# Kernel tuning notes

Hardware: AMD Instinct MI355X
Metric: run time of the kernel (lower is better)

Reference implementation:

```python
import jax, jax.numpy as jnp
import numpy as np

HIDDEN = 1024
HEADS = 16
HEAD_DIM = HIDDEN // HEADS


def setup_inputs() -> dict:
    key = jax.random.key(0)
    ks = jax.random.split(key, 8)
    B, S = 4, 2048
    scale = 1.0 / np.sqrt(HIDDEN)
    return {
        "hidden_states": jax.random.normal(ks[0], (B, S, HIDDEN), dtype=jnp.float32),
        "attention_mask": jnp.zeros((B, 1, 1, S), dtype=jnp.float32),
        "Wq": jax.random.normal(ks[1], (HIDDEN, HIDDEN), dtype=jnp.float32) * scale,
        "bq": jnp.zeros((HIDDEN,), dtype=jnp.float32),
        "Wk": jax.random.normal(ks[2], (HIDDEN, HIDDEN), dtype=jnp.float32) * scale,
        "bk": jnp.zeros((HIDDEN,), dtype=jnp.float32),
        "Wv": jax.random.normal(ks[3], (HIDDEN, HIDDEN), dtype=jnp.float32) * scale,
        "bv": jnp.zeros((HIDDEN,), dtype=jnp.float32),
    }


def _split_heads(x):
    # [B, S, H] -> [B, heads, S, d]
    B, S, _ = x.shape
    return x.reshape(B, S, HEADS, HEAD_DIM).transpose(0, 2, 1, 3)


def reference(hidden_states, attention_mask, Wq, bq, Wk, bk, Wv, bv):
    # nn.Linear: y = x @ W.T + b
    q = _split_heads(hidden_states @ Wq.T + bq)
    k = _split_heads(hidden_states @ Wk.T + bk)
    v = _split_heads(hidden_states @ Wv.T + bv)
    scores = jnp.einsum("bhqd,bhkd->bhqk", q, k) / np.sqrt(HEAD_DIM)
    scores = scores + attention_mask  # additive broadcast mask
    probs = jax.nn.softmax(scores, axis=-1)
    # dropout is identity in eval mode (deterministic reference)
    ctx = jnp.einsum("bhqk,bhkd->bhqd", probs, v)
    B, _, S, _ = ctx.shape
    ctx = ctx.transpose(0, 2, 1, 3).reshape(B, S, HIDDEN)
    return ctx, probs
```

## Files before the change

kernel.cpp:

```cpp
#include <hip/hip_runtime.h>
#include <cstdint>
#include <cstddef>


#define BB 4
#define SS 2048
#define HID 1024
#define NH 16
#define HD 64
#define MTOT (BB * SS)
#define BH (BB * NH)

__global__ __launch_bounds__(256) void qkv_gemm(const float* __restrict__ X,
                                                const float* __restrict__ W,
                                                const float* __restrict__ bias,
                                                float* __restrict__ out) {
    __shared__ float As[16][68];
    __shared__ float Bs[16][68];
    const int t  = threadIdx.x;
    const int m0 = blockIdx.y * 64;
    const int n0 = blockIdx.x * 64;
    const int lr = t >> 2;
    const int lc = (t & 3) * 4;
    const int tr = (t >> 4) * 4;
    const int tc = (t & 15) * 4;

    float acc[4][4];
#pragma unroll
    for (int u = 0; u < 4; u++)
#pragma unroll
        for (int v = 0; v < 4; v++) acc[u][v] = 0.f;

    const float* Xp = X + (size_t)(m0 + lr) * HID + lc;
    const float* Wp = W + (size_t)(n0 + lr) * HID + lc;

    for (int k0 = 0; k0 < HID; k0 += 16) {
        float4 a = *(const float4*)(Xp + k0);
        float4 b = *(const float4*)(Wp + k0);
        __syncthreads();
        As[lc + 0][lr] = a.x; As[lc + 1][lr] = a.y; As[lc + 2][lr] = a.z; As[lc + 3][lr] = a.w;
        Bs[lc + 0][lr] = b.x; Bs[lc + 1][lr] = b.y; Bs[lc + 2][lr] = b.z; Bs[lc + 3][lr] = b.w;
        __syncthreads();
#pragma unroll
        for (int kk = 0; kk < 16; kk++) {
            float4 av = *(const float4*)&As[kk][tr];
            float4 bv = *(const float4*)&Bs[kk][tc];
            acc[0][0] += av.x * bv.x; acc[0][1] += av.x * bv.y; acc[0][2] += av.x * bv.z; acc[0][3] += av.x * bv.w;
            acc[1][0] += av.y * bv.x; acc[1][1] += av.y * bv.y; acc[1][2] += av.y * bv.z; acc[1][3] += av.y * bv.w;
            acc[2][0] += av.z * bv.x; acc[2][1] += av.z * bv.y; acc[2][2] += av.z * bv.z; acc[2][3] += av.z * bv.w;
            acc[3][0] += av.w * bv.x; acc[3][1] += av.w * bv.y; acc[3][2] += av.w * bv.z; acc[3][3] += av.w * bv.w;
        }
    }

    const int n_base = n0 + tc;
    const int h  = n_base >> 6;
    const int d0 = n_base & 63;
    const float4 bvec = *(const float4*)&bias[n_base];
#pragma unroll
    for (int u = 0; u < 4; u++) {
        const int m = m0 + tr + u;
        const int bb = m >> 11;
        const int s  = m & (SS - 1);
        float4 r;
        r.x = acc[u][0] + bvec.x; r.y = acc[u][1] + bvec.y;
        r.z = acc[u][2] + bvec.z; r.w = acc[u][3] + bvec.w;
        *(float4*)&out[((size_t)(bb * NH + h) * SS + s) * HD + d0] = r;
    }
}

__global__ __launch_bounds__(256) void attn(const float* __restrict__ Q,
                                            const float* __restrict__ K,
                                            const float* __restrict__ V,
                                            const float* __restrict__ mask,
                                            float* __restrict__ probs,
                                            float* __restrict__ ctx,
                                            float* __restrict__ invZ) {
    const int bh = blockIdx.x;
    const int q0 = blockIdx.y * 32;
    const int b  = bh >> 4;
    const int h  = bh & 15;
    const int t  = threadIdx.x;

    __shared__ float q_lds[32][68];
    __shared__ float kT[64][68];
    __shared__ float v_lds[64][68];
    __shared__ float e_lds[32][68];
    __shared__ float m_lds[64];

    {
        const int r = t >> 3, c0 = (t & 7) * 8;
        const float* gq = Q + ((size_t)bh * SS + q0 + r) * HD + c0;
        *(float4*)&q_lds[r][c0]     = *(const float4*)gq;
        *(float4*)&q_lds[r][c0 + 4] = *(const float4*)(gq + 4);
    }

    const int i  = t >> 3;
    const int jc = (t & 7) * 4;

    float ctx_acc[8];
#pragma unroll
    for (int u = 0; u < 8; u++) ctx_acc[u] = 0.f;
    float Zpart = 0.f;

    const float* Kb    = K + (size_t)bh * SS * HD;
    const float* Vb    = V + (size_t)bh * SS * HD;
    const float* maskb = mask + (size_t)b * SS;
    float* probs_row   = probs + ((size_t)bh * SS + q0 + i) * SS;

    const int lr = t >> 2;
    const int lc0 = (t & 3) * 16;

    for (int kt = 0; kt < SS; kt += 64) {
        __syncthreads();
        {
            const float* kg = Kb + (size_t)(kt + lr) * HD + lc0;
            const float* vg = Vb + (size_t)(kt + lr) * HD + lc0;
#pragma unroll
            for (int ii = 0; ii < 4; ii++) {
                float4 kx = *(const float4*)(kg + ii * 4);
                kT[lc0 + ii * 4 + 0][lr] = kx.x;
                kT[lc0 + ii * 4 + 1][lr] = kx.y;
                kT[lc0 + ii * 4 + 2][lr] = kx.z;
                kT[lc0 + ii * 4 + 3][lr] = kx.w;
                *(float4*)&v_lds[lr][lc0 + ii * 4] = *(const float4*)(vg + ii * 4);
            }
            if (t < 64) m_lds[t] = maskb[kt + t];
        }
        __syncthreads();

        float sA[4] = {0.f, 0.f, 0.f, 0.f}, sB[4] = {0.f, 0.f, 0.f, 0.f};
#pragma unroll 8
        for (int c = 0; c < 64; c++) {
            const float qv = q_lds[i][c];
            const float4 ka = *(const float4*)&kT[c][jc];
            const float4 kb = *(const float4*)&kT[c][jc + 32];
            sA[0] += qv * ka.x; sA[1] += qv * ka.y; sA[2] += qv * ka.z; sA[3] += qv * ka.w;
            sB[0] += qv * kb.x; sB[1] += qv * kb.y; sB[2] += qv * kb.z; sB[3] += qv * kb.w;
        }
        float4 eA, eB;
        eA.x = __expf(sA[0] * 0.125f + m_lds[jc + 0]);
        eA.y = __expf(sA[1] * 0.125f + m_lds[jc + 1]);
        eA.z = __expf(sA[2] * 0.125f + m_lds[jc + 2]);
        eA.w = __expf(sA[3] * 0.125f + m_lds[jc + 3]);
        eB.x = __expf(sB[0] * 0.125f + m_lds[jc + 32]);
        eB.y = __expf(sB[1] * 0.125f + m_lds[jc + 33]);
        eB.z = __expf(sB[2] * 0.125f + m_lds[jc + 34]);
        eB.w = __expf(sB[3] * 0.125f + m_lds[jc + 35]);
        Zpart += eA.x + eA.y + eA.z + eA.w + eB.x + eB.y + eB.z + eB.w;
        *(float4*)&e_lds[i][jc]      = eA;
        *(float4*)&e_lds[i][jc + 32] = eB;
        *(float4*)(probs_row + kt + jc)      = eA;
        *(float4*)(probs_row + kt + jc + 32) = eB;
        __syncthreads();

#pragma unroll 8
        for (int j = 0; j < 64; j++) {
            const float ev = e_lds[i][j];
            const float4 va = *(const float4*)&v_lds[j][jc];
            const float4 vb = *(const float4*)&v_lds[j][jc + 32];
            ctx_acc[0] += ev * va.x; ctx_acc[1] += ev * va.y; ctx_acc[2] += ev * va.z; ctx_acc[3] += ev * va.w;
            ctx_acc[4] += ev * vb.x; ctx_acc[5] += ev * vb.y; ctx_acc[6] += ev * vb.z; ctx_acc[7] += ev * vb.w;
        }
    }

    Zpart += __shfl_xor(Zpart, 1);
    Zpart += __shfl_xor(Zpart, 2);
    Zpart += __shfl_xor(Zpart, 4);
    const float inv = 1.0f / Zpart;
    if ((t & 7) == 0) invZ[(size_t)bh * SS + q0 + i] = inv;

    float* gc = ctx + ((size_t)b * SS + q0 + i) * HID + h * HD;
    float4 ra, rb;
    ra.x = ctx_acc[0] * inv; ra.y = ctx_acc[1] * inv; ra.z = ctx_acc[2] * inv; ra.w = ctx_acc[3] * inv;
    rb.x = ctx_acc[4] * inv; rb.y = ctx_acc[5] * inv; rb.z = ctx_acc[6] * inv; rb.w = ctx_acc[7] * inv;
    *(float4*)(gc + jc)      = ra;
    *(float4*)(gc + jc + 32) = rb;
}

__global__ __launch_bounds__(256) void rescale(float* __restrict__ probs,
                                               const float* __restrict__ invZ) {
    const size_t total4 = (size_t)BH * SS * SS / 4;
    const size_t stride = (size_t)gridDim.x * 256;
    for (size_t p = (size_t)blockIdx.x * 256 + threadIdx.x; p < total4; p += stride) {
        const size_t row = p >> 9;
        const float iz = invZ[row];
        float4 v = ((const float4*)probs)[p];
        v.x *= iz; v.y *= iz; v.z *= iz; v.w *= iz;
        ((float4*)probs)[p] = v;
    }
}

extern "C" void kernel_launch(void* const* d_in, const int* in_sizes, int n_in,
                              void* d_out, int out_size, void* d_ws, size_t ws_size,
                              hipStream_t stream) {
    const float* hs   = (const float*)d_in[0];
    const float* mask = (const float*)d_in[1];
    const float* Wq   = (const float*)d_in[2];
    const float* bq   = (const float*)d_in[3];
    const float* Wk   = (const float*)d_in[4];
    const float* bk   = (const float*)d_in[5];
    const float* Wv   = (const float*)d_in[6];
    const float* bv   = (const float*)d_in[7];

    float* ctx   = (float*)d_out;
    float* probs = (float*)d_out + (size_t)BB * SS * HID;

    const size_t qkv_elems = (size_t)BH * SS * HD;
    float* Qw   = (float*)d_ws;
    float* Kw   = Qw + qkv_elems;
    float* Vw   = Kw + qkv_elems;
    float* invZ = Vw + qkv_elems;
    (void)ws_size; (void)in_sizes; (void)n_in; (void)out_size;

    dim3 gproj(HID / 64, MTOT / 64);
    qkv_gemm<<<gproj, 256, 0, stream>>>(hs, Wq, bq, Qw);
    qkv_gemm<<<gproj, 256, 0, stream>>>(hs, Wk, bk, Kw);
    qkv_gemm<<<gproj, 256, 0, stream>>>(hs, Wv, bv, Vw);

    dim3 gattn(BH, SS / 32);
    attn<<<gattn, 256, 0, stream>>>(Qw, Kw, Vw, mask, probs, ctx, invZ);

    rescale<<<32768, 256, 0, stream>>>(probs, invZ);
}
```

Measured before the change: 3.434 ms.

## Use split-bf16 MFMA for attention QK and PV products

The projection GEMM now writes Q, K and V as hi/lo bf16 pairs, with V stored transposed. The scalar-FP32 attention kernel is replaced by one that computes QK^T and P·V with 16x16x32 bf16 MFMA instructions. Three products per pair (hi·hi, hi·lo, lo·hi) approximate fp32 accuracy. This removes the scalar FMA cost of the attention matmuls at the price of extra split arithmetic, LDS traffic for P, and uncoalesced strided probs stores.

```diff
diff --git a/kernel.cpp b/kernel.cpp
--- a/kernel.cpp
+++ b/kernel.cpp
@@ -11,10 +11,33 @@
 #define MTOT (BB * SS)
 #define BH (BB * NH)
 
+typedef __attribute__((ext_vector_type(8))) short sv8;
+typedef __attribute__((ext_vector_type(4))) float fv4;
+
+__device__ __forceinline__ fv4 mfma16(sv8 a, sv8 b, fv4 c) {
+    return __builtin_amdgcn_mfma_f32_16x16x32_bf16(a, b, c, 0, 0, 0);
+}
+
+__device__ __forceinline__ ushort bf16_rn(float x) {
+    union { float f; unsigned u; } v; v.f = x;
+    const unsigned r = v.u + 0x7FFFu + ((v.u >> 16) & 1u);
+    return (ushort)(r >> 16);
+}
+__device__ __forceinline__ float bf16_f(ushort h) {
+    union { unsigned u; float f; } v; v.u = ((unsigned)h) << 16;
+    return v.f;
+}
+__device__ __forceinline__ void split2(float x, ushort& hi, ushort& lo) {
+    hi = bf16_rn(x);
+    lo = bf16_rn(x - bf16_f(hi));
+}
+
 __global__ __launch_bounds__(256) void qkv_gemm(const float* __restrict__ X,
                                                 const float* __restrict__ W,
                                                 const float* __restrict__ bias,
-                                                float* __restrict__ out) {
+                                                ushort* __restrict__ outH,
+                                                ushort* __restrict__ outL,
+                                                const int vtrans) {
     __shared__ float As[16][68];
     __shared__ float Bs[16][68];
     const int t  = threadIdx.x;
@@ -56,125 +79,168 @@
     const int h  = n_base >> 6;
     const int d0 = n_base & 63;
     const float4 bvec = *(const float4*)&bias[n_base];
-#pragma unroll
-    for (int u = 0; u < 4; u++) {
-        const int m = m0 + tr + u;
+    const float bv4[4] = {bvec.x, bvec.y, bvec.z, bvec.w};
+
+    if (!vtrans) {
+#pragma unroll
+        for (int u = 0; u < 4; u++) {
+            const int m  = m0 + tr + u;
+            const int bb = m >> 11;
+            const int s  = m & (SS - 1);
+            ushort4 hq, lq;
+            split2(acc[u][0] + bv4[0], hq.x, lq.x);
+            split2(acc[u][1] + bv4[1], hq.y, lq.y);
+            split2(acc[u][2] + bv4[2], hq.z, lq.z);
+            split2(acc[u][3] + bv4[3], hq.w, lq.w);
+            const size_t off = ((size_t)(bb * NH + h) * SS + s) * HD + d0;
+            *(ushort4*)&outH[off] = hq;
+            *(ushort4*)&outL[off] = lq;
+        }
+    } else {
+        const int m  = m0 + tr;
         const int bb = m >> 11;
         const int s  = m & (SS - 1);
-        float4 r;
-        r.x = acc[u][0] + bvec.x; r.y = acc[u][1] + bvec.y;
-        r.z = acc[u][2] + bvec.z; r.w = acc[u][3] + bvec.w;
-        *(float4*)&out[((size_t)(bb * NH + h) * SS + s) * HD + d0] = r;
-    }
-}
-
-__global__ __launch_bounds__(256) void attn(const float* __restrict__ Q,
-                                            const float* __restrict__ K,
-                                            const float* __restrict__ V,
-                                            const float* __restrict__ mask,
-                                            float* __restrict__ probs,
-                                            float* __restrict__ ctx,
-                                            float* __restrict__ invZ) {
+#pragma unroll
+        for (int v = 0; v < 4; v++) {
+            ushort4 hq, lq;
+            split2(acc[0][v] + bv4[v], hq.x, lq.x);
+            split2(acc[1][v] + bv4[v], hq.y, lq.y);
+            split2(acc[2][v] + bv4[v], hq.z, lq.z);
+            split2(acc[3][v] + bv4[v], hq.w, lq.w);
+            const size_t off = ((size_t)(bb * NH + h) * HD + (d0 + v)) * SS + s;
+            *(ushort4*)&outH[off] = hq;
+            *(ushort4*)&outL[off] = lq;
+        }
+    }
+}
+
+__global__ __launch_bounds__(256) void attn_mfma(const ushort* __restrict__ Qh, const ushort* __restrict__ Ql,
+                                                 const ushort* __restrict__ Kh, const ushort* __restrict__ Kl,
+                                                 const ushort* __restrict__ Vth, const ushort* __restrict__ Vtl,
+                                                 const float* __restrict__ mask,
+                                                 float* __restrict__ probs,
+                                                 float* __restrict__ ctx,
+                                                 float* __restrict__ invZ) {
     const int bh = blockIdx.x;
     const int q0 = blockIdx.y * 32;
     const int b  = bh >> 4;
-    const int h  = bh & 15;
+    const int hh = bh & 15;
     const int t  = threadIdx.x;
-
-    __shared__ float q_lds[32][68];
-    __shared__ float kT[64][68];
-    __shared__ float v_lds[64][68];
-    __shared__ float e_lds[32][68];
-    __shared__ float m_lds[64];
-
-    {
-        const int r = t >> 3, c0 = (t & 7) * 8;
-        const float* gq = Q + ((size_t)bh * SS + q0 + r) * HD + c0;
-        *(float4*)&q_lds[r][c0]     = *(const float4*)gq;
-        *(float4*)&q_lds[r][c0 + 4] = *(const float4*)(gq + 4);
-    }
-
-    const int i  = t >> 3;
-    const int jc = (t & 7) * 4;
-
-    float ctx_acc[8];
-#pragma unroll
-    for (int u = 0; u < 8; u++) ctx_acc[u] = 0.f;
-    float Zpart = 0.f;
-
-    const float* Kb    = K + (size_t)bh * SS * HD;
-    const float* Vb    = V + (size_t)bh * SS * HD;
+    const int w   = t >> 6;
+    const int l   = t & 63;
+    const int m16 = l & 15;
+    const int g   = l >> 4;
+    const int qb  = w & 1;
+    const int c2  = w >> 1;
+
+    __shared__ __attribute__((aligned(16))) ushort Ph[32][72];
+    __shared__ __attribute__((aligned(16))) ushort Pl[32][72];
+    __shared__ float zsl[2][2][16];
+
+    const size_t qoff = ((size_t)bh * SS + q0 + qb * 16 + m16) * HD + 8 * g;
+    const sv8 qh0 = *(const sv8*)(Qh + qoff);
+    const sv8 qh1 = *(const sv8*)(Qh + qoff + 32);
+    const sv8 ql0 = *(const sv8*)(Ql + qoff);
+    const sv8 ql1 = *(const sv8*)(Ql + qoff + 32);
+
+    fv4 cacc0 = {0.f, 0.f, 0.f, 0.f};
+    fv4 cacc1 = {0.f, 0.f, 0.f, 0.f};
+    float zp[4] = {0.f, 0.f, 0.f, 0.f};
+
     const float* maskb = mask + (size_t)b * SS;
-    float* probs_row   = probs + ((size_t)bh * SS + q0 + i) * SS;
-
-    const int lr = t >> 2;
-    const int lc0 = (t & 3) * 16;
 
     for (int kt = 0; kt < SS; kt += 64) {
-        __syncthreads();
-        {
-            const float* kg = Kb + (size_t)(kt + lr) * HD + lc0;
-            const float* vg = Vb + (size_t)(kt + lr) * HD + lc0;
-#pragma unroll
-            for (int ii = 0; ii < 4; ii++) {
-                float4 kx = *(const float4*)(kg + ii * 4);
-                kT[lc0 + ii * 4 + 0][lr] = kx.x;
-                kT[lc0 + ii * 4 + 1][lr] = kx.y;
-                kT[lc0 + ii * 4 + 2][lr] = kx.z;
-                kT[lc0 + ii * 4 + 3][lr] = kx.w;
-                *(float4*)&v_lds[lr][lc0 + ii * 4] = *(const float4*)(vg + ii * 4);
+#pragma unroll
+        for (int x = 0; x < 2; x++) {
+            const int kb   = c2 * 2 + x;
+            const int krow = kt + kb * 16 + m16;
+            const size_t koff = ((size_t)bh * SS + krow) * HD + 8 * g;
+            const sv8 kh0 = *(const sv8*)(Kh + koff);
+            const sv8 kh1 = *(const sv8*)(Kh + koff + 32);
+            const sv8 kl0 = *(const sv8*)(Kl + koff);
+            const sv8 kl1 = *(const sv8*)(Kl + koff + 32);
+            fv4 s = {0.f, 0.f, 0.f, 0.f};
+            s = mfma16(qh0, kh0, s);
+            s = mfma16(qh1, kh1, s);
+            s = mfma16(qh0, kl0, s);
+            s = mfma16(qh1, kl1, s);
+            s = mfma16(ql0, kh0, s);
+            s = mfma16(ql1, kh1, s);
+
+            const float mv = maskb[krow];
+            float* prow = probs + ((size_t)bh * SS + q0 + qb * 16 + 4 * g) * SS + krow;
+#pragma unroll
+            for (int r = 0; r < 4; r++) {
+                const float e = __expf(s[r] * 0.125f + mv);
+                zp[r] += e;
+                prow[(size_t)r * SS] = e;
+                ushort hi, lo;
+                split2(e, hi, lo);
+                Ph[qb * 16 + 4 * g + r][kb * 16 + m16] = hi;
+                Pl[qb * 16 + 4 * g + r][kb * 16 + m16] = lo;
             }
-            if (t < 64) m_lds[t] = maskb[kt + t];
-        }
-        __syncthreads();
-
-        float sA[4] = {0.f, 0.f, 0.f, 0.f}, sB[4] = {0.f, 0.f, 0.f, 0.f};
-#pragma unroll 8
-        for (int c = 0; c < 64; c++) {
-            const float qv = q_lds[i][c];
-            const float4 ka = *(const float4*)&kT[c][jc];
-            const float4 kb = *(const float4*)&kT[c][jc + 32];
-            sA[0] += qv * ka.x; sA[1] += qv * ka.y; sA[2] += qv * ka.z; sA[3] += qv * ka.w;
-            sB[0] += qv * kb.x; sB[1] += qv * kb.y; sB[2] += qv * kb.z; sB[3] += qv * kb.w;
-        }
-        float4 eA, eB;
-        eA.x = __expf(sA[0] * 0.125f + m_lds[jc + 0]);
-        eA.y = __expf(sA[1] * 0.125f + m_lds[jc + 1]);
-        eA.z = __expf(sA[2] * 0.125f + m_lds[jc + 2]);
-        eA.w = __expf(sA[3] * 0.125f + m_lds[jc + 3]);
-        eB.x = __expf(sB[0] * 0.125f + m_lds[jc + 32]);
-        eB.y = __expf(sB[1] * 0.125f + m_lds[jc + 33]);
-        eB.z = __expf(sB[2] * 0.125f + m_lds[jc + 34]);
-        eB.w = __expf(sB[3] * 0.125f + m_lds[jc + 35]);
-        Zpart += eA.x + eA.y + eA.z + eA.w + eB.x + eB.y + eB.z + eB.w;
-        *(float4*)&e_lds[i][jc]      = eA;
-        *(float4*)&e_lds[i][jc + 32] = eB;
-        *(float4*)(probs_row + kt + jc)      = eA;
-        *(float4*)(probs_row + kt + jc + 32) = eB;
-        __syncthreads();
-
-#pragma unroll 8
-        for (int j = 0; j < 64; j++) {
-            const float ev = e_lds[i][j];
-            const float4 va = *(const float4*)&v_lds[j][jc];
-            const float4 vb = *(const float4*)&v_lds[j][jc + 32];
-            ctx_acc[0] += ev * va.x; ctx_acc[1] += ev * va.y; ctx_acc[2] += ev * va.z; ctx_acc[3] += ev * va.w;
-            ctx_acc[4] += ev * vb.x; ctx_acc[5] += ev * vb.y; ctx_acc[6] += ev * vb.z; ctx_acc[7] += ev * vb.w;
-        }
-    }
-
-    Zpart += __shfl_xor(Zpart, 1);
-    Zpart += __shfl_xor(Zpart, 2);
-    Zpart += __shfl_xor(Zpart, 4);
-    const float inv = 1.0f / Zpart;
-    if ((t & 7) == 0) invZ[(size_t)bh * SS + q0 + i] = inv;
-
-    float* gc = ctx + ((size_t)b * SS + q0 + i) * HID + h * HD;
-    float4 ra, rb;
-    ra.x = ctx_acc[0] * inv; ra.y = ctx_acc[1] * inv; ra.z = ctx_acc[2] * inv; ra.w = ctx_acc[3] * inv;
-    rb.x = ctx_acc[4] * inv; rb.y = ctx_acc[5] * inv; rb.z = ctx_acc[6] * inv; rb.w = ctx_acc[7] * inv;
-    *(float4*)(gc + jc)      = ra;
-    *(float4*)(gc + jc + 32) = rb;
+        }
+        __syncthreads();
+
+        const ushort* phr = &Ph[qb * 16 + m16][0];
+        const ushort* plr = &Pl[qb * 16 + m16][0];
+        const sv8 ph0 = *(const sv8*)(phr + 8 * g);
+        const sv8 ph1 = *(const sv8*)(phr + 8 * g + 32);
+        const sv8 pl0 = *(const sv8*)(plr + 8 * g);
+        const sv8 pl1 = *(const sv8*)(plr + 8 * g + 32);
+#pragma unroll
+        for (int x = 0; x < 2; x++) {
+            const int db = c2 * 2 + x;
+            const size_t voff = ((size_t)bh * HD + db * 16 + m16) * SS + kt + 8 * g;
+            const sv8 vh0 = *(const sv8*)(Vth + voff);
+            const sv8 vh1 = *(const sv8*)(Vth + voff + 32);
+            const sv8 vl0 = *(const sv8*)(Vtl + voff);
+            const sv8 vl1 = *(const sv8*)(Vtl + voff + 32);
+            fv4 c = x ? cacc1 : cacc0;
+            c = mfma16(ph0, vh0, c);
+            c = mfma16(ph1, vh1, c);
+            c = mfma16(ph0, vl0, c);
+            c = mfma16(ph1, vl1, c);
+            c = mfma16(pl0, vh0, c);
+            c = mfma16(pl1, vh1, c);
+            if (x) cacc1 = c; else cacc0 = c;
+        }
+        __syncthreads();
+    }
+
+#pragma unroll
+    for (int r = 0; r < 4; r++) {
+        zp[r] += __shfl_xor(zp[r], 1);
+        zp[r] += __shfl_xor(zp[r], 2);
+        zp[r] += __shfl_xor(zp[r], 4);
+        zp[r] += __shfl_xor(zp[r], 8);
+    }
+    if (m16 == 0) {
+#pragma unroll
+        for (int r = 0; r < 4; r++) zsl[c2][qb][4 * g + r] = zp[r];
+    }
+    __syncthreads();
+    float inv[4];
+#pragma unroll
+    for (int r = 0; r < 4; r++) {
+        const int row = 4 * g + r;
+        inv[r] = 1.0f / (zsl[0][qb][row] + zsl[1][qb][row]);
+    }
+    if (c2 == 0 && m16 == 0) {
+#pragma unroll
+        for (int r = 0; r < 4; r++) invZ[(size_t)bh * SS + q0 + qb * 16 + 4 * g + r] = inv[r];
+    }
+
+    float* cb = ctx + ((size_t)b * SS + q0 + qb * 16 + 4 * g) * HID + hh * HD + m16;
+#pragma unroll
+    for (int x = 0; x < 2; x++) {
+        const int db = c2 * 2 + x;
+        const fv4 c = x ? cacc1 : cacc0;
+#pragma unroll
+        for (int r = 0; r < 4; r++) {
+            cb[(size_t)r * HID + db * 16] = c[r] * inv[r];
+        }
+    }
 }
 
 __global__ __launch_bounds__(256) void rescale(float* __restrict__ probs,
@@ -206,19 +272,22 @@
     float* probs = (float*)d_out + (size_t)BB * SS * HID;
 
     const size_t qkv_elems = (size_t)BH * SS * HD;
-    float* Qw   = (float*)d_ws;
-    float* Kw   = Qw + qkv_elems;
-    float* Vw   = Kw + qkv_elems;
-    float* invZ = Vw + qkv_elems;
+    ushort* Qh = (ushort*)d_ws;
+    ushort* Ql = Qh + qkv_elems;
+    ushort* Kh = Ql + qkv_elems;
+    ushort* Kl = Kh + qkv_elems;
+    ushort* Vh = Kl + qkv_elems;
+    ushort* Vl = Vh + qkv_elems;
+    float* invZ = (float*)(Vl + qkv_elems);
     (void)ws_size; (void)in_sizes; (void)n_in; (void)out_size;
 
     dim3 gproj(HID / 64, MTOT / 64);
-    qkv_gemm<<<gproj, 256, 0, stream>>>(hs, Wq, bq, Qw);
-    qkv_gemm<<<gproj, 256, 0, stream>>>(hs, Wk, bk, Kw);
-    qkv_gemm<<<gproj, 256, 0, stream>>>(hs, Wv, bv, Vw);
+    qkv_gemm<<<gproj, 256, 0, stream>>>(hs, Wq, bq, Qh, Ql, 0);
+    qkv_gemm<<<gproj, 256, 0, stream>>>(hs, Wk, bk, Kh, Kl, 0);
+    qkv_gemm<<<gproj, 256, 0, stream>>>(hs, Wv, bv, Vh, Vl, 1);
 
     dim3 gattn(BH, SS / 32);
-    attn<<<gattn, 256, 0, stream>>>(Qw, Kw, Vw, mask, probs, ctx, invZ);
+    attn_mfma<<<gattn, 256, 0, stream>>>(Qh, Ql, Kh, Kl, Vh, Vl, mask, probs, ctx, invZ);
 
     rescale<<<32768, 256, 0, stream>>>(probs, invZ);
 }
```

After: 3.512 ms. 1.02x slower.
